# Kernel optimization log

Measured on AMD Instinct MI355X. Metric: run time of the kernel, lower is better.

The kernel has to match this reference:

```python
import jax, jax.numpy as jnp
import numpy as np

N_HEAD = 4

def setup_inputs() -> dict:
    key = jax.random.key(0)
    ks = jax.random.split(key, 5)
    B, T, C = 2, 4096, 64
    return {
        "x": jax.random.normal(ks[0], (B, T, C), dtype=jnp.float32),
        "w_attn": jax.random.normal(ks[1], (3 * C, C), dtype=jnp.float32) * 0.02,
        "b_attn": jax.random.normal(ks[2], (3 * C,), dtype=jnp.float32) * 0.02,
        "w_proj": jax.random.normal(ks[3], (C, C), dtype=jnp.float32) * 0.02,
        "b_proj": jax.random.normal(ks[4], (C,), dtype=jnp.float32) * 0.02,
    }

def reference(x, w_attn, b_attn, w_proj, b_proj):
    B, T, C = x.shape
    H = N_HEAD
    Dh = C // H
    # fused QKV projection (torch Linear: x @ W.T + b)
    qkv = x @ w_attn.T + b_attn                      # [B,T,3C]
    q, k, v = jnp.split(qkv, 3, axis=-1)             # each [B,T,C]
    q = q.reshape(B, T, H, Dh).transpose(0, 2, 1, 3)  # [B,H,T,Dh]
    k = k.reshape(B, T, H, Dh).transpose(0, 2, 1, 3)
    v = v.reshape(B, T, H, Dh).transpose(0, 2, 1, 3)
    scale = 1.0 / np.sqrt(Dh).astype(np.float32)
    scores = jnp.einsum("bhqd,bhkd->bhqk", q, k) * scale  # [B,H,T,T]
    attn = jax.nn.softmax(scores, axis=-1)
    y = jnp.einsum("bhqk,bhkd->bhqd", attn, v)       # [B,H,T,Dh]
    y = y.transpose(0, 2, 1, 3).reshape(B, T, C)     # [B,T,C]
    return y @ w_proj.T + b_proj
```

## Files before the change

### kernel.cpp

```cpp
#include <hip/hip_runtime.h>
#include <math.h>

#define BB 2
#define TT 4096
#define CC 64
#define HH 4
#define DH 16
#define NROW (BB*TT)
#define SCALE 0.36067376022224085f

typedef __fp16 h4 __attribute__((ext_vector_type(4)));
typedef __fp16 h2 __attribute__((ext_vector_type(2)));
typedef float  f4 __attribute__((ext_vector_type(4)));


union U32B { struct { uint4 a, b; } u; h4 f[4]; };
__device__ __forceinline__ U32B ld32(const __fp16* p) {
    U32B r;
    r.u.a = *(const uint4*)p;
    r.u.b = *(const uint4*)(p + 8);
    return r;
}

__global__ __launch_bounds__(256) void qkv_kernel(const float* __restrict__ x,
        const float* __restrict__ w, const float* __restrict__ bias,
        __fp16* __restrict__ Q, __fp16* __restrict__ K, __fp16* __restrict__ VT) {
    __shared__ __fp16 smv[64][16];
    const int t = threadIdx.x;
    const int wave = t >> 6, lane = t & 63;
    const int lq = lane & 15, g = lane >> 4;
    const int r0 = blockIdx.x*16;
    const int b = r0 >> 12, tt0 = r0 & (TT-1);
    const int chunk = tt0 >> 6, seg = (tt0 >> 4) & 3;

    h4 xb[4];
    const float* xrow = x + (size_t)(r0 + lq)*CC;
    #pragma unroll
    for (int s = 0; s < 4; s++) {
        float4 xv = *(const float4*)(xrow + s*16 + g*4);
        h2 lo = __builtin_amdgcn_cvt_pkrtz(xv.x, xv.y);
        h2 hi = __builtin_amdgcn_cvt_pkrtz(xv.z, xv.w);
        xb[s] = (h4){lo.x, lo.y, hi.x, hi.y};
    }

    #pragma unroll
    for (int j = 0; j < 3; j++) {
        const int nt = wave*3 + j;
        const int o0 = nt*16;
        const float sc = (nt < 4) ? SCALE : 1.0f;
        float4 bv = *(const float4*)(bias + o0 + g*4);
        f4 acc = {bv.x*sc, bv.y*sc, bv.z*sc, bv.w*sc};
        #pragma unroll
        for (int s = 0; s < 4; s++) {
            float4 wv = *(const float4*)(w + (size_t)(o0 + lq)*CC + s*16 + g*4);
            h2 lo = __builtin_amdgcn_cvt_pkrtz(wv.x*sc, wv.y*sc);
            h2 hi = __builtin_amdgcn_cvt_pkrtz(wv.z*sc, wv.w*sc);
            h4 af = (h4){lo.x, lo.y, hi.x, hi.y};
            acc = __builtin_amdgcn_mfma_f32_16x16x16f16(af, xb[s], acc, 0, 0, 0);
        }
        h2 plo = __builtin_amdgcn_cvt_pkrtz(acc.x, acc.y);
        h2 phi = __builtin_amdgcn_cvt_pkrtz(acc.z, acc.w);
        h4 pk = (h4){plo.x, plo.y, phi.x, phi.y};
        if (nt < 8) {
            const int part = nt >> 2, h = nt & 3;
            __fp16* dst = ((part == 0) ? Q : K)
                + (size_t)(b*HH + h)*(TT*DH) + chunk*1024 + lane*16 + seg*4;
            *(h4*)dst = pk;
        } else {
            const int h = nt - 8;
            smv[h*16 + g*4 + 0][lq] = pk.x;
            smv[h*16 + g*4 + 1][lq] = pk.y;
            smv[h*16 + g*4 + 2][lq] = pk.z;
            smv[h*16 + g*4 + 3][lq] = pk.w;
        }
    }
    __syncthreads();
    {
        const int h = t >> 6, n = t & 63;
        h4 vv = *(const h4*)&smv[h*16 + (n & 15)][(n >> 4)*4];
        __fp16* dst = VT + (size_t)(b*HH + h)*(TT*DH) + chunk*1024 + n*16 + seg*4;
        *(h4*)dst = vv;
    }
}

__global__ __launch_bounds__(256) void attn_kernel(const __fp16* __restrict__ Q,
        const __fp16* __restrict__ K, const __fp16* __restrict__ VT,
        __fp16* __restrict__ yh) {
    __shared__ f4    Osm[4][4][64];
    __shared__ float Lsm[4][4][64];
    const int t = threadIdx.x;
    const int wave = t >> 6, lane = t & 63;
    const int lq = lane & 15, g = lane >> 4;
    const int head = blockIdx.x >> 6;
    const int qt   = blockIdx.x & 63;
    const int q0 = qt*64;
    const __fp16* Qh = Q  + (size_t)head*TT*DH;
    const __fp16* Kh = K  + (size_t)head*TT*DH;
    const __fp16* Vh = VT + (size_t)head*TT*DH;

    U32B qfu = ld32(Qh + (size_t)qt*1024 + lane*16);

    f4 O[4];
    float lp[4];
    #pragma unroll
    for (int h = 0; h < 4; h++) { O[h] = (f4){0.f,0.f,0.f,0.f}; lp[h] = 0.f; }

    const __fp16* kbase = Kh + (size_t)(wave*16)*1024 + lane*16;
    const __fp16* vbase = Vh + (size_t)(wave*16)*1024 + lane*16;

    U32B ka = ld32(kbase), va = ld32(vbase);
    U32B kb, vb;

#define ATTN_CHUNK(KF, VF)                                                        \
    {                                                                             \
        const f4 z = {0.f, 0.f, 0.f, 0.f};                                        \
        _Pragma("unroll")                                                         \
        for (int h = 0; h < 4; h++) {                                             \
            f4 S0 = __builtin_amdgcn_mfma_f32_16x16x16f16(KF.f[0], qfu.f[h], z, 0,0,0);\
            f4 S1 = __builtin_amdgcn_mfma_f32_16x16x16f16(KF.f[1], qfu.f[h], z, 0,0,0);\
            f4 S2 = __builtin_amdgcn_mfma_f32_16x16x16f16(KF.f[2], qfu.f[h], z, 0,0,0);\
            f4 S3 = __builtin_amdgcn_mfma_f32_16x16x16f16(KF.f[3], qfu.f[h], z, 0,0,0);\
            float p0, p1, p2, p3; h2 lo, hi; h4 P; float lacc = 0.f;              \
            p0 = __builtin_amdgcn_exp2f(S0.x); p1 = __builtin_amdgcn_exp2f(S0.y); \
            p2 = __builtin_amdgcn_exp2f(S0.z); p3 = __builtin_amdgcn_exp2f(S0.w); \
            lacc += p0 + p1 + p2 + p3;                                            \
            lo = __builtin_amdgcn_cvt_pkrtz(p0, p1);                              \
            hi = __builtin_amdgcn_cvt_pkrtz(p2, p3);                              \
            P = (h4){lo.x, lo.y, hi.x, hi.y};                                     \
            O[h] = __builtin_amdgcn_mfma_f32_16x16x16f16(VF.f[0], P, O[h], 0,0,0);\
            p0 = __builtin_amdgcn_exp2f(S1.x); p1 = __builtin_amdgcn_exp2f(S1.y); \
            p2 = __builtin_amdgcn_exp2f(S1.z); p3 = __builtin_amdgcn_exp2f(S1.w); \
            lacc += p0 + p1 + p2 + p3;                                            \
            lo = __builtin_amdgcn_cvt_pkrtz(p0, p1);                              \
            hi = __builtin_amdgcn_cvt_pkrtz(p2, p3);                              \
            P = (h4){lo.x, lo.y, hi.x, hi.y};                                     \
            O[h] = __builtin_amdgcn_mfma_f32_16x16x16f16(VF.f[1], P, O[h], 0,0,0);\
            p0 = __builtin_amdgcn_exp2f(S2.x); p1 = __builtin_amdgcn_exp2f(S2.y); \
            p2 = __builtin_amdgcn_exp2f(S2.z); p3 = __builtin_amdgcn_exp2f(S2.w); \
            lacc += p0 + p1 + p2 + p3;                                            \
            lo = __builtin_amdgcn_cvt_pkrtz(p0, p1);                              \
            hi = __builtin_amdgcn_cvt_pkrtz(p2, p3);                              \
            P = (h4){lo.x, lo.y, hi.x, hi.y};                                     \
            O[h] = __builtin_amdgcn_mfma_f32_16x16x16f16(VF.f[2], P, O[h], 0,0,0);\
            p0 = __builtin_amdgcn_exp2f(S3.x); p1 = __builtin_amdgcn_exp2f(S3.y); \
            p2 = __builtin_amdgcn_exp2f(S3.z); p3 = __builtin_amdgcn_exp2f(S3.w); \
            lacc += p0 + p1 + p2 + p3;                                            \
            lo = __builtin_amdgcn_cvt_pkrtz(p0, p1);                              \
            hi = __builtin_amdgcn_cvt_pkrtz(p2, p3);                              \
            P = (h4){lo.x, lo.y, hi.x, hi.y};                                     \
            O[h] = __builtin_amdgcn_mfma_f32_16x16x16f16(VF.f[3], P, O[h], 0,0,0);\
            lp[h] += lacc;                                                        \
        }                                                                         \
    }

    for (int it = 0; it < 16; it += 2) {
        kb = ld32(kbase + (size_t)(it + 1)*1024);
        vb = ld32(vbase + (size_t)(it + 1)*1024);
        ATTN_CHUNK(ka, va)
        {
            const int c2 = (it + 2 < 16) ? it + 2 : 15;
            ka = ld32(kbase + (size_t)c2*1024);
            va = ld32(vbase + (size_t)c2*1024);
        }
        ATTN_CHUNK(kb, vb)
    }
#undef ATTN_CHUNK

    #pragma unroll
    for (int h = 0; h < 4; h++) {
        Osm[wave][h][lane] = O[h];
        Lsm[wave][h][lane] = lp[h];
    }
    __syncthreads();

    f4 Os = Osm[0][wave][lane];
    Os += Osm[1][wave][lane];
    Os += Osm[2][wave][lane];
    Os += Osm[3][wave][lane];
    float L = 0.f;
    #pragma unroll
    for (int ks = 0; ks < 4; ks++)
        #pragma unroll
        for (int gg = 0; gg < 4; gg++)
            L += Lsm[ks][wave][gg*16 + lq];
    const float rinv = 1.f / L;
    h2 lo = __builtin_amdgcn_cvt_pkrtz(Os.x*rinv, Os.y*rinv);
    h2 hi = __builtin_amdgcn_cvt_pkrtz(Os.z*rinv, Os.w*rinv);
    h4 pk = (h4){lo.x, lo.y, hi.x, hi.y};
    const int b = head >> 2, hh = head & 3;
    const size_t rblk = ((size_t)b*TT + q0) / 16 + wave;
    *(h4*)(yh + rblk*1024 + lane*16 + hh*4) = pk;
}

__global__ __launch_bounds__(256) void proj_kernel(const __fp16* __restrict__ yh,
        const float* __restrict__ w, const float* __restrict__ bias,
        float* __restrict__ out) {
    const int t = threadIdx.x;
    const int wave = t >> 6, lane = t & 63;
    const int lq = lane & 15, g = lane >> 4;
    const int r0 = blockIdx.x*16;
    const int o0 = wave*16;

    U32B yb = ld32(yh + (size_t)blockIdx.x*1024 + lane*16);

    float4 bv = *(const float4*)(bias + o0 + g*4);
    f4 acc = {bv.x, bv.y, bv.z, bv.w};
    #pragma unroll
    for (int s = 0; s < 4; s++) {
        float4 wv = *(const float4*)(w + (size_t)(o0 + lq)*CC + s*16 + g*4);
        h2 lo = __builtin_amdgcn_cvt_pkrtz(wv.x, wv.y);
        h2 hi = __builtin_amdgcn_cvt_pkrtz(wv.z, wv.w);
        h4 af = (h4){lo.x, lo.y, hi.x, hi.y};
        acc = __builtin_amdgcn_mfma_f32_16x16x16f16(af, yb.f[s], acc, 0, 0, 0);
    }
    *(float4*)(out + (size_t)(r0 + lq)*CC + o0 + g*4) = (float4){acc.x, acc.y, acc.z, acc.w};
}

extern "C" void kernel_launch(void* const* d_in, const int* in_sizes, int n_in,
                              void* d_out, int out_size, void* d_ws, size_t ws_size,
                              hipStream_t stream) {
    const float* x      = (const float*)d_in[0];
    const float* w_attn = (const float*)d_in[1];
    const float* b_attn = (const float*)d_in[2];
    const float* w_proj = (const float*)d_in[3];
    const float* b_proj = (const float*)d_in[4];
    float* out = (float*)d_out;

    const size_t headsz = (size_t)BB*HH*TT*DH;
    __fp16* Q   = (__fp16*)d_ws;
    __fp16* K   = Q + headsz;
    __fp16* VT  = K + headsz;
    __fp16* yh  = VT + headsz;

    qkv_kernel<<<NROW/16, 256, 0, stream>>>(x, w_attn, b_attn, Q, K, VT);
    attn_kernel<<<BB*HH*(TT/64), 256, 0, stream>>>(Q, K, VT, yh);
    proj_kernel<<<NROW/16, 256, 0, stream>>>(yh, w_proj, b_proj, out);
}
```

Measured before the change: 96.26 us.

## Fuse QKV, attention and projection into one persistent kernel with grid barriers

```diff
diff --git a/kernel.cpp b/kernel.cpp
--- a/kernel.cpp
+++ b/kernel.cpp
@@ -7,12 +7,12 @@
 #define HH 4
 #define DH 16
 #define NROW (BB*TT)
+#define NBLK 512
 #define SCALE 0.36067376022224085f
 
 typedef __fp16 h4 __attribute__((ext_vector_type(4)));
 typedef __fp16 h2 __attribute__((ext_vector_type(2)));
 typedef float  f4 __attribute__((ext_vector_type(4)));
-
 
 union U32B { struct { uint4 a, b; } u; h4 f[4]; };
 __device__ __forceinline__ U32B ld32(const __fp16* p) {
@@ -22,94 +22,108 @@
     return r;
 }
 
-__global__ __launch_bounds__(256) void qkv_kernel(const float* __restrict__ x,
-        const float* __restrict__ w, const float* __restrict__ bias,
-        __fp16* __restrict__ Q, __fp16* __restrict__ K, __fp16* __restrict__ VT) {
-    __shared__ __fp16 smv[64][16];
+__device__ __forceinline__ void grid_barrier(unsigned* cnt) {
+    __syncthreads();
+    if (threadIdx.x == 0) {
+        __threadfence();
+        __hip_atomic_fetch_add(cnt, 1u, __ATOMIC_RELEASE, __HIP_MEMORY_SCOPE_AGENT);
+        while (__hip_atomic_load(cnt, __ATOMIC_ACQUIRE, __HIP_MEMORY_SCOPE_AGENT) < (unsigned)NBLK)
+            __builtin_amdgcn_s_sleep(2);
+    }
+    __syncthreads();
+}
+
+__global__ __launch_bounds__(256) void fused_kernel(const float* __restrict__ x,
+        const float* __restrict__ w_attn, const float* __restrict__ b_attn,
+        const float* __restrict__ w_proj, const float* __restrict__ b_proj,
+        __fp16* __restrict__ Q, __fp16* __restrict__ K, __fp16* __restrict__ VT,
+        __fp16* __restrict__ yh, float* __restrict__ out, unsigned* __restrict__ bar) {
+    __shared__ __align__(16) char smraw[20480];
     const int t = threadIdx.x;
+    const int bid = blockIdx.x;
     const int wave = t >> 6, lane = t & 63;
     const int lq = lane & 15, g = lane >> 4;
-    const int r0 = blockIdx.x*16;
-    const int b = r0 >> 12, tt0 = r0 & (TT-1);
-    const int chunk = tt0 >> 6, seg = (tt0 >> 4) & 3;
-
-    h4 xb[4];
-    const float* xrow = x + (size_t)(r0 + lq)*CC;
-    #pragma unroll
-    for (int s = 0; s < 4; s++) {
-        float4 xv = *(const float4*)(xrow + s*16 + g*4);
-        h2 lo = __builtin_amdgcn_cvt_pkrtz(xv.x, xv.y);
-        h2 hi = __builtin_amdgcn_cvt_pkrtz(xv.z, xv.w);
-        xb[s] = (h4){lo.x, lo.y, hi.x, hi.y};
-    }
-
-    #pragma unroll
-    for (int j = 0; j < 3; j++) {
-        const int nt = wave*3 + j;
-        const int o0 = nt*16;
-        const float sc = (nt < 4) ? SCALE : 1.0f;
-        float4 bv = *(const float4*)(bias + o0 + g*4);
-        f4 acc = {bv.x*sc, bv.y*sc, bv.z*sc, bv.w*sc};
+
+    {
+        __fp16 (*smv)[16] = (__fp16(*)[16])smraw;
+        const int r0 = bid*16;
+        const int b = r0 >> 12, tt0 = r0 & (TT-1);
+        const int chunk = tt0 >> 6, seg = (tt0 >> 4) & 3;
+
+        h4 xb[4];
+        const float* xrow = x + (size_t)(r0 + lq)*CC;
         #pragma unroll
         for (int s = 0; s < 4; s++) {
-            float4 wv = *(const float4*)(w + (size_t)(o0 + lq)*CC + s*16 + g*4);
-            h2 lo = __builtin_amdgcn_cvt_pkrtz(wv.x*sc, wv.y*sc);
-            h2 hi = __builtin_amdgcn_cvt_pkrtz(wv.z*sc, wv.w*sc);
-            h4 af = (h4){lo.x, lo.y, hi.x, hi.y};
-            acc = __builtin_amdgcn_mfma_f32_16x16x16f16(af, xb[s], acc, 0, 0, 0);
-        }
-        h2 plo = __builtin_amdgcn_cvt_pkrtz(acc.x, acc.y);
-        h2 phi = __builtin_amdgcn_cvt_pkrtz(acc.z, acc.w);
-        h4 pk = (h4){plo.x, plo.y, phi.x, phi.y};
-        if (nt < 8) {
-            const int part = nt >> 2, h = nt & 3;
-            __fp16* dst = ((part == 0) ? Q : K)
-                + (size_t)(b*HH + h)*(TT*DH) + chunk*1024 + lane*16 + seg*4;
-            *(h4*)dst = pk;
-        } else {
-            const int h = nt - 8;
-            smv[h*16 + g*4 + 0][lq] = pk.x;
-            smv[h*16 + g*4 + 1][lq] = pk.y;
-            smv[h*16 + g*4 + 2][lq] = pk.z;
-            smv[h*16 + g*4 + 3][lq] = pk.w;
-        }
-    }
-    __syncthreads();
+            float4 xv = *(const float4*)(xrow + s*16 + g*4);
+            h2 lo = __builtin_amdgcn_cvt_pkrtz(xv.x, xv.y);
+            h2 hi = __builtin_amdgcn_cvt_pkrtz(xv.z, xv.w);
+            xb[s] = (h4){lo.x, lo.y, hi.x, hi.y};
+        }
+
+        #pragma unroll
+        for (int j = 0; j < 3; j++) {
+            const int nt = wave*3 + j;
+            const int o0 = nt*16;
+            const float sc = (nt < 4) ? SCALE : 1.0f;
+            float4 bv = *(const float4*)(b_attn + o0 + g*4);
+            f4 acc = {bv.x*sc, bv.y*sc, bv.z*sc, bv.w*sc};
+            #pragma unroll
+            for (int s = 0; s < 4; s++) {
+                float4 wv = *(const float4*)(w_attn + (size_t)(o0 + lq)*CC + s*16 + g*4);
+                h2 lo = __builtin_amdgcn_cvt_pkrtz(wv.x*sc, wv.y*sc);
+                h2 hi = __builtin_amdgcn_cvt_pkrtz(wv.z*sc, wv.w*sc);
+                h4 af = (h4){lo.x, lo.y, hi.x, hi.y};
+                acc = __builtin_amdgcn_mfma_f32_16x16x16f16(af, xb[s], acc, 0, 0, 0);
+            }
+            h2 plo = __builtin_amdgcn_cvt_pkrtz(acc.x, acc.y);
+            h2 phi = __builtin_amdgcn_cvt_pkrtz(acc.z, acc.w);
+            h4 pk = (h4){plo.x, plo.y, phi.x, phi.y};
+            if (nt < 8) {
+                const int part = nt >> 2, h = nt & 3;
+                __fp16* dst = ((part == 0) ? Q : K)
+                    + (size_t)(b*HH + h)*(TT*DH) + chunk*1024 + lane*16 + seg*4;
+                *(h4*)dst = pk;
+            } else {
+                const int h = nt - 8;
+                smv[h*16 + g*4 + 0][lq] = pk.x;
+                smv[h*16 + g*4 + 1][lq] = pk.y;
+                smv[h*16 + g*4 + 2][lq] = pk.z;
+                smv[h*16 + g*4 + 3][lq] = pk.w;
+            }
+        }
+        __syncthreads();
+        {
+            const int h = t >> 6, n = t & 63;
+            h4 vv = *(const h4*)&smv[h*16 + (n & 15)][(n >> 4)*4];
+            __fp16* dst = VT + (size_t)(b*HH + h)*(TT*DH) + chunk*1024 + n*16 + seg*4;
+            *(h4*)dst = vv;
+        }
+    }
+
+    grid_barrier(&bar[0]);
+
     {
-        const int h = t >> 6, n = t & 63;
-        h4 vv = *(const h4*)&smv[h*16 + (n & 15)][(n >> 4)*4];
-        __fp16* dst = VT + (size_t)(b*HH + h)*(TT*DH) + chunk*1024 + n*16 + seg*4;
-        *(h4*)dst = vv;
-    }
-}
-
-__global__ __launch_bounds__(256) void attn_kernel(const __fp16* __restrict__ Q,
-        const __fp16* __restrict__ K, const __fp16* __restrict__ VT,
-        __fp16* __restrict__ yh) {
-    __shared__ f4    Osm[4][4][64];
-    __shared__ float Lsm[4][4][64];
-    const int t = threadIdx.x;
-    const int wave = t >> 6, lane = t & 63;
-    const int lq = lane & 15, g = lane >> 4;
-    const int head = blockIdx.x >> 6;
-    const int qt   = blockIdx.x & 63;
-    const int q0 = qt*64;
-    const __fp16* Qh = Q  + (size_t)head*TT*DH;
-    const __fp16* Kh = K  + (size_t)head*TT*DH;
-    const __fp16* Vh = VT + (size_t)head*TT*DH;
-
-    U32B qfu = ld32(Qh + (size_t)qt*1024 + lane*16);
-
-    f4 O[4];
-    float lp[4];
-    #pragma unroll
-    for (int h = 0; h < 4; h++) { O[h] = (f4){0.f,0.f,0.f,0.f}; lp[h] = 0.f; }
-
-    const __fp16* kbase = Kh + (size_t)(wave*16)*1024 + lane*16;
-    const __fp16* vbase = Vh + (size_t)(wave*16)*1024 + lane*16;
-
-    U32B ka = ld32(kbase), va = ld32(vbase);
-    U32B kb, vb;
+        f4    (*Osm)[4][64] = (f4(*)[4][64])smraw;
+        float (*Lsm)[4][64] = (float(*)[4][64])(smraw + 16384);
+        const int head = bid >> 6;
+        const int qt   = bid & 63;
+        const int q0 = qt*64;
+        const __fp16* Qh = Q  + (size_t)head*TT*DH;
+        const __fp16* Kh = K  + (size_t)head*TT*DH;
+        const __fp16* Vh = VT + (size_t)head*TT*DH;
+
+        U32B qfu = ld32(Qh + (size_t)qt*1024 + lane*16);
+
+        f4 O[4];
+        float lp[4];
+        #pragma unroll
+        for (int h = 0; h < 4; h++) { O[h] = (f4){0.f,0.f,0.f,0.f}; lp[h] = 0.f; }
+
+        const __fp16* kbase = Kh + (size_t)(wave*16)*1024 + lane*16;
+        const __fp16* vbase = Vh + (size_t)(wave*16)*1024 + lane*16;
+
+        U32B ka = ld32(kbase), va = ld32(vbase);
+        U32B kb, vb;
 
 #define ATTN_CHUNK(KF, VF)                                                        \
     {                                                                             \
@@ -153,67 +167,66 @@
         }                                                                         \
     }
 
-    for (int it = 0; it < 16; it += 2) {
-        kb = ld32(kbase + (size_t)(it + 1)*1024);
-        vb = ld32(vbase + (size_t)(it + 1)*1024);
-        ATTN_CHUNK(ka, va)
-        {
-            const int c2 = (it + 2 < 16) ? it + 2 : 15;
-            ka = ld32(kbase + (size_t)c2*1024);
-            va = ld32(vbase + (size_t)c2*1024);
-        }
-        ATTN_CHUNK(kb, vb)
-    }
+        for (int it = 0; it < 16; it += 2) {
+            kb = ld32(kbase + (size_t)(it + 1)*1024);
+            vb = ld32(vbase + (size_t)(it + 1)*1024);
+            ATTN_CHUNK(ka, va)
+            {
+                const int c2 = (it + 2 < 16) ? it + 2 : 15;
+                ka = ld32(kbase + (size_t)c2*1024);
+                va = ld32(vbase + (size_t)c2*1024);
+            }
+            ATTN_CHUNK(kb, vb)
+        }
 #undef ATTN_CHUNK
 
-    #pragma unroll
-    for (int h = 0; h < 4; h++) {
-        Osm[wave][h][lane] = O[h];
-        Lsm[wave][h][lane] = lp[h];
-    }
-    __syncthreads();
-
-    f4 Os = Osm[0][wave][lane];
-    Os += Osm[1][wave][lane];
-    Os += Osm[2][wave][lane];
-    Os += Osm[3][wave][lane];
-    float L = 0.f;
-    #pragma unroll
-    for (int ks = 0; ks < 4; ks++)
-        #pragma unroll
-        for (int gg = 0; gg < 4; gg++)
-            L += Lsm[ks][wave][gg*16 + lq];
-    const float rinv = 1.f / L;
-    h2 lo = __builtin_amdgcn_cvt_pkrtz(Os.x*rinv, Os.y*rinv);
-    h2 hi = __builtin_amdgcn_cvt_pkrtz(Os.z*rinv, Os.w*rinv);
-    h4 pk = (h4){lo.x, lo.y, hi.x, hi.y};
-    const int b = head >> 2, hh = head & 3;
-    const size_t rblk = ((size_t)b*TT + q0) / 16 + wave;
-    *(h4*)(yh + rblk*1024 + lane*16 + hh*4) = pk;
-}
-
-__global__ __launch_bounds__(256) void proj_kernel(const __fp16* __restrict__ yh,
-        const float* __restrict__ w, const float* __restrict__ bias,
-        float* __restrict__ out) {
-    const int t = threadIdx.x;
-    const int wave = t >> 6, lane = t & 63;
-    const int lq = lane & 15, g = lane >> 4;
-    const int r0 = blockIdx.x*16;
-    const int o0 = wave*16;
-
-    U32B yb = ld32(yh + (size_t)blockIdx.x*1024 + lane*16);
-
-    float4 bv = *(const float4*)(bias + o0 + g*4);
-    f4 acc = {bv.x, bv.y, bv.z, bv.w};
-    #pragma unroll
-    for (int s = 0; s < 4; s++) {
-        float4 wv = *(const float4*)(w + (size_t)(o0 + lq)*CC + s*16 + g*4);
-        h2 lo = __builtin_amdgcn_cvt_pkrtz(wv.x, wv.y);
-        h2 hi = __builtin_amdgcn_cvt_pkrtz(wv.z, wv.w);
-        h4 af = (h4){lo.x, lo.y, hi.x, hi.y};
-        acc = __builtin_amdgcn_mfma_f32_16x16x16f16(af, yb.f[s], acc, 0, 0, 0);
-    }
-    *(float4*)(out + (size_t)(r0 + lq)*CC + o0 + g*4) = (float4){acc.x, acc.y, acc.z, acc.w};
+        __syncthreads();
+        #pragma unroll
+        for (int h = 0; h < 4; h++) {
+            Osm[wave][h][lane] = O[h];
+            Lsm[wave][h][lane] = lp[h];
+        }
+        __syncthreads();
+
+        f4 Os = Osm[0][wave][lane];
+        Os += Osm[1][wave][lane];
+        Os += Osm[2][wave][lane];
+        Os += Osm[3][wave][lane];
+        float L = 0.f;
+        #pragma unroll
+        for (int ks = 0; ks < 4; ks++)
+            #pragma unroll
+            for (int gg = 0; gg < 4; gg++)
+                L += Lsm[ks][wave][gg*16 + lq];
+        const float rinv = 1.f / L;
+        h2 lo = __builtin_amdgcn_cvt_pkrtz(Os.x*rinv, Os.y*rinv);
+        h2 hi = __builtin_amdgcn_cvt_pkrtz(Os.z*rinv, Os.w*rinv);
+        h4 pk = (h4){lo.x, lo.y, hi.x, hi.y};
+        const int b = head >> 2, hh = head & 3;
+        const size_t rblk = ((size_t)b*TT + q0) / 16 + wave;
+        *(h4*)(yh + rblk*1024 + lane*16 + hh*4) = pk;
+    }
+
+    grid_barrier(&bar[1]);
+
+    {
+        const int r0 = bid*16;
+        const int o0 = wave*16;
+
+        U32B yb = ld32(yh + (size_t)bid*1024 + lane*16);
+
+        float4 bv = *(const float4*)(b_proj + o0 + g*4);
+        f4 acc = {bv.x, bv.y, bv.z, bv.w};
+        #pragma unroll
+        for (int s = 0; s < 4; s++) {
+            float4 wv = *(const float4*)(w_proj + (size_t)(o0 + lq)*CC + s*16 + g*4);
+            h2 lo = __builtin_amdgcn_cvt_pkrtz(wv.x, wv.y);
+            h2 hi = __builtin_amdgcn_cvt_pkrtz(wv.z, wv.w);
+            h4 af = (h4){lo.x, lo.y, hi.x, hi.y};
+            acc = __builtin_amdgcn_mfma_f32_16x16x16f16(af, yb.f[s], acc, 0, 0, 0);
+        }
+        *(float4*)(out + (size_t)(r0 + lq)*CC + o0 + g*4) = (float4){acc.x, acc.y, acc.z, acc.w};
+    }
 }
 
 extern "C" void kernel_launch(void* const* d_in, const int* in_sizes, int n_in,
@@ -231,8 +244,9 @@
     __fp16* K   = Q + headsz;
     __fp16* VT  = K + headsz;
     __fp16* yh  = VT + headsz;
-
-    qkv_kernel<<<NROW/16, 256, 0, stream>>>(x, w_attn, b_attn, Q, K, VT);
-    attn_kernel<<<BB*HH*(TT/64), 256, 0, stream>>>(Q, K, VT, yh);
-    proj_kernel<<<NROW/16, 256, 0, stream>>>(yh, w_proj, b_proj, out);
-}
+    unsigned* bar = (unsigned*)((char*)d_ws + (16u << 20));
+
+    hipMemsetAsync(bar, 0, 16, stream);
+    fused_kernel<<<NBLK, 256, 0, stream>>>(x, w_attn, b_attn, w_proj, b_proj,
+                                           Q, K, VT, yh, out, bar);
+}
```

Result: slower. 218.6 us (+127.1%).
